# Kernel tuning notes

Hardware: AMD Instinct MI355X
Metric: run time of the kernel (lower is better)

## Reference

```python
import jax, jax.numpy as jnp
import numpy as np
import math

NEG = -1000000.0


def setup_inputs() -> dict:
    key = jax.random.key(0)
    ks = jax.random.split(key, 8)
    B, S, D = 4, 2048, 1024
    std = 1.0 / math.sqrt(D)
    return {
        "queries": jax.random.normal(ks[0], (B, S, D), jnp.float32),
        "keys": jax.random.normal(ks[1], (B, S, D), jnp.float32),
        "values": jax.random.normal(ks[2], (B, S, D), jnp.float32),
        "valid_len": jax.random.randint(ks[3], (B,), 1, S, dtype=jnp.int64 if jax.config.jax_enable_x64 else jnp.int32),
        "W_q": jax.random.normal(ks[4], (D, D), jnp.float32) * std,
        "W_k": jax.random.normal(ks[5], (D, D), jnp.float32) * std,
        "W_v": jax.random.normal(ks[6], (D, D), jnp.float32) * std,
        "W_o": jax.random.normal(ks[7], (D, D), jnp.float32) * std,
    }


def reference(queries, keys, values, valid_len, W_q, W_k, W_v, W_o):
    NUM_HEADS = 16
    B, S, D = queries.shape
    hd = D // NUM_HEADS

    def split_heads(x):
        # (B, S, D) -> (B, H, S, hd)
        return x.reshape(B, -1, NUM_HEADS, hd).transpose(0, 2, 1, 3)

    # nn.Linear with weight W applies x @ W.T
    q = split_heads(queries @ W_q.T)
    k = split_heads(keys @ W_k.T)
    v = split_heads(values @ W_v.T)

    scale = 1.0 / math.sqrt(hd)
    scores = jnp.einsum('bhqd,bhkd->bhqk', q, k) * scale  # (B, H, Sq, Sk)

    # key-padding mask from valid_len: positions >= valid_len are masked
    kpos = jnp.arange(scores.shape[-1])
    pad_mask = kpos[None, None, None, :] >= valid_len[:, None, None, None]
    scores = jnp.where(pad_mask, NEG, scores)
    attn = jax.nn.softmax(scores, axis=-1)

    out = jnp.einsum('bhqk,bhkd->bhqd', attn, v)  # (B, H, Sq, hd)
    out = out.transpose(0, 2, 1, 3).reshape(B, -1, D)
    return out @ W_o.T
```

## Files before the change

kernel.cpp:

```cpp
#include <hip/hip_runtime.h>
#include <hip/hip_bf16.h>

using bf16_t = __bf16;
using bf16x8 = __attribute__((ext_vector_type(8))) __bf16;
using bf16x4 = __attribute__((ext_vector_type(4))) __bf16;
using bf16x2 = __attribute__((ext_vector_type(2))) __bf16;
using f32x4  = __attribute__((ext_vector_type(4))) float;

#define S_  2048
#define D_  1024

typedef __attribute__((address_space(1))) unsigned int glb_u32;
typedef __attribute__((address_space(3))) unsigned int lds_u32;

__device__ __forceinline__ void async_cp16(const void* g, void* lds) {
    __builtin_amdgcn_global_load_lds(
        (glb_u32*)(unsigned long long)g,
        (lds_u32*)(unsigned int)(unsigned long long)lds,
        16, 0, 0);
}

__global__ __launch_bounds__(256) void cast_f32_bf16(const float* __restrict__ s,
                                                     bf16_t* __restrict__ d, int n4) {
    int i = blockIdx.x * 256 + threadIdx.x;
    if (i >= n4) return;
    float4 f = reinterpret_cast<const float4*>(s)[i];
    bf16x4 o;
    o[0] = (bf16_t)f.x; o[1] = (bf16_t)f.y; o[2] = (bf16_t)f.z; o[3] = (bf16_t)f.w;
    reinterpret_cast<bf16x4*>(d)[i] = o;
}

__global__ __launch_bounds__(256) void cast2_f32_bf16(const float* __restrict__ a, const float* __restrict__ b,
                                                      bf16_t* __restrict__ oa, bf16_t* __restrict__ ob, int n4) {
    int i = blockIdx.x * 256 + threadIdx.x;
    if (i >= n4) return;
    const float* s = blockIdx.y ? b : a;
    bf16_t*      d = blockIdx.y ? ob : oa;
    float4 f = reinterpret_cast<const float4*>(s)[i];
    bf16x4 o;
    o[0] = (bf16_t)f.x; o[1] = (bf16_t)f.y; o[2] = (bf16_t)f.z; o[3] = (bf16_t)f.w;
    reinterpret_cast<bf16x4*>(d)[i] = o;
}

__global__ __launch_bounds__(256) void cast4_f32_bf16(const float* __restrict__ a, const float* __restrict__ b,
                                                      const float* __restrict__ c, const float* __restrict__ dd,
                                                      bf16_t* __restrict__ oa, bf16_t* __restrict__ ob,
                                                      bf16_t* __restrict__ oc, bf16_t* __restrict__ od, int n4) {
    int i = blockIdx.x * 256 + threadIdx.x;
    if (i >= n4) return;
    const float* s; bf16_t* d;
    int w = blockIdx.y;
    if      (w == 0) { s = a;  d = oa; }
    else if (w == 1) { s = b;  d = ob; }
    else if (w == 2) { s = c;  d = oc; }
    else             { s = dd; d = od; }
    float4 f = reinterpret_cast<const float4*>(s)[i];
    bf16x4 o;
    o[0] = (bf16_t)f.x; o[1] = (bf16_t)f.y; o[2] = (bf16_t)f.z; o[3] = (bf16_t)f.w;
    reinterpret_cast<bf16x4*>(d)[i] = o;
}

template <int OUTMODE>
__global__ __launch_bounds__(256) void gemm_bt(const bf16_t* __restrict__ A,
                                               const bf16_t* __restrict__ Bt,
                                               void* __restrict__ Cv, float scale) {
    __shared__ bf16_t As[128 * 32];
    __shared__ bf16_t Bs[128 * 32];
    const int K = 1024;
    int tid  = threadIdx.x;
    int lane = tid & 63;
    int w    = tid >> 6;
    int l15  = lane & 15, quad = lane >> 4;
    int m0 = blockIdx.y * 128, n0 = blockIdx.x * 128;
    int wm = (w >> 1) * 64, wn = (w & 1) * 64;

    const bf16_t* Ag = A  + (size_t)(m0 + (tid >> 2)) * K + (tid & 3) * 8;
    const bf16_t* Bg = Bt + (size_t)(n0 + (tid >> 2)) * K + (tid & 3) * 8;
    bf16_t* Asw = As + tid * 8;
    bf16_t* Bsw = Bs + tid * 8;

    f32x4 acc[4][4] = {};

    for (int k0 = 0; k0 < K; k0 += 32) {
        __syncthreads();
        async_cp16(Ag + k0,                    Asw);
        async_cp16(Ag + k0 + (size_t)64 * K,   Asw + 2048);
        async_cp16(Bg + k0,                    Bsw);
        async_cp16(Bg + k0 + (size_t)64 * K,   Bsw + 2048);
        __syncthreads();
        bf16x8 af[4], bfr[4];
#pragma unroll
        for (int t = 0; t < 4; t++) {
            af[t]  = *reinterpret_cast<const bf16x8*>(&As[(wm + t * 16 + l15) * 32 + quad * 8]);
            bfr[t] = *reinterpret_cast<const bf16x8*>(&Bs[(wn + t * 16 + l15) * 32 + quad * 8]);
        }
#pragma unroll
        for (int mt = 0; mt < 4; mt++)
#pragma unroll
            for (int nt = 0; nt < 4; nt++)
                acc[mt][nt] = __builtin_amdgcn_mfma_f32_16x16x32_bf16(af[mt], bfr[nt], acc[mt][nt], 0, 0, 0);
    }

#pragma unroll
    for (int mt = 0; mt < 4; mt++)
#pragma unroll
        for (int nt = 0; nt < 4; nt++) {
            if (OUTMODE == 2) {
                int m = m0 + wm + mt * 16 + quad * 4;
                int n = n0 + wn + nt * 16 + l15;
                bf16x4 o4;
#pragma unroll
                for (int r = 0; r < 4; r++) o4[r] = (bf16_t)(acc[mt][nt][r] * scale);
                size_t vrow = (size_t)((m >> 11) * 16 + (n >> 6)) * 64 + (n & 63);
                *reinterpret_cast<bf16x4*>(&((bf16_t*)Cv)[vrow * S_ + (m & 2047)]) = o4;
            } else {
#pragma unroll
                for (int r = 0; r < 4; r++) {
                    int m = m0 + wm + mt * 16 + quad * 4 + r;
                    int n = n0 + wn + nt * 16 + l15;
                    size_t idx = (size_t)m * 1024 + n;
                    if (OUTMODE == 1) reinterpret_cast<float*>(Cv)[idx] = acc[mt][nt][r] * scale;
                    else              reinterpret_cast<bf16_t*>(Cv)[idx] = (bf16_t)(acc[mt][nt][r] * scale);
                }
            }
        }
}

__global__ __launch_bounds__(256) void attn_fused(const bf16_t* __restrict__ Qp,
                                                  const bf16_t* __restrict__ Kp,
                                                  const bf16_t* __restrict__ Vt,
                                                  const int* __restrict__ vlen_p,
                                                  bf16_t* __restrict__ Out) {
    __shared__ bf16_t smem[4][64 * 64];

    int tid  = threadIdx.x;
    int lane = tid & 63, w = tid >> 6;
    int l15  = lane & 15, quad = lane >> 4;

    int nk[4], ord[4] = {0, 1, 2, 3};
#pragma unroll
    for (int i = 0; i < 4; i++) nk[i] = (vlen_p[i] + 63) >> 6;
#pragma unroll
    for (int i = 0; i < 3; i++)
#pragma unroll
        for (int j = 0; j < 3 - i; j++)
            if (nk[ord[j + 1]] > nk[ord[j]]) { int t = ord[j]; ord[j] = ord[j + 1]; ord[j + 1] = t; }

    int bid  = blockIdx.x;
    int b    = ord[bid >> 9];
    int t    = bid & 511;
    int h    = (t & 7) * 2 + ((t >> 3) & 1);
    int qblk = t >> 4;
    int vlen = vlen_p[b];
    int nkb  = (vlen + 63) >> 6;

    const bf16_t* Qg = Qp + (size_t)(b * S_ + qblk * 64) * D_ + h * 64;
    const bf16_t* Kg = Kp + (size_t)b * S_ * D_ + h * 64;
    const bf16_t* Vg = Vt + (size_t)(b * 16 + h) * 64 * S_;

    auto stage = [&](const bf16_t* g, size_t rstride, bf16_t* lds) {
#pragma unroll
        for (int j = 0; j < 2; j++) {
            int linear = j * 256 + tid;
            int row = linear >> 3, s = linear & 7;
            async_cp16(g + (size_t)row * rstride + (s ^ (row & 7)) * 8, lds + linear * 8);
        }
    };

    stage(Qg, D_, smem[2]);
    stage(Kg, D_, smem[0]);
    stage(Vg, S_, smem[1]);
    __syncthreads();

    bf16x8 qf[2];
    {
        int row = w * 16 + l15, x = row & 7;
#pragma unroll
        for (int kk = 0; kk < 2; kk++)
            qf[kk] = *reinterpret_cast<const bf16x8*>(&smem[2][row * 64 + ((kk * 4 + quad) ^ x) * 8]);
    }
    __syncthreads();

    f32x4 o[4] = {};
    float l_st = 0.f;

    for (int kb = 0; kb < nkb; kb++) {
        int cur = kb & 1;
        if (kb + 1 < nkb) {
            int nxt = cur ^ 1;
            stage(Kg + (size_t)(kb + 1) * 64 * D_, D_, smem[nxt * 2]);
            stage(Vg + (kb + 1) * 64,              S_, smem[nxt * 2 + 1]);
        }
        const bf16_t* Kc = smem[cur * 2];
        const bf16_t* Vc = smem[cur * 2 + 1];

        f32x4 sc[4] = {};
#pragma unroll
        for (int nt = 0; nt < 4; nt++) {
            int row = nt * 16 + l15, x = row & 7;
#pragma unroll
            for (int kk = 0; kk < 2; kk++) {
                bf16x8 kf = *reinterpret_cast<const bf16x8*>(&Kc[row * 64 + ((kk * 4 + quad) ^ x) * 8]);
                sc[nt] = __builtin_amdgcn_mfma_f32_16x16x32_bf16(kf, qf[kk], sc[nt], 0, 0, 0);
            }
        }

        bool partial = (vlen & 63) && (kb == nkb - 1);
        bf16x8 pf[2];
        float lacc = 0.f;
        if (!partial) {
#pragma unroll
            for (int nt = 0; nt < 4; nt++)
#pragma unroll
                for (int r = 0; r < 4; r++) {
                    float p = __builtin_exp2f(sc[nt][r]);
                    lacc += p;
                    pf[nt >> 1][(nt & 1) * 4 + r] = (bf16_t)p;
                }
        } else {
#pragma unroll
            for (int nt = 0; nt < 4; nt++)
#pragma unroll
                for (int r = 0; r < 4; r++) {
                    float p = __builtin_exp2f(sc[nt][r]);
                    if (kb * 64 + nt * 16 + quad * 4 + r >= vlen) p = 0.f;
                    lacc += p;
                    pf[nt >> 1][(nt & 1) * 4 + r] = (bf16_t)p;
                }
        }
        l_st += lacc;

#pragma unroll
        for (int np = 0; np < 2; np++)
#pragma unroll
            for (int dt = 0; dt < 4; dt++) {
                int row = dt * 16 + l15, x = row & 7;
                int off = (quad & 1) * 4;
                bf16x4 v0 = *reinterpret_cast<const bf16x4*>(&Vc[row * 64 + (((np * 4)     + (quad >> 1)) ^ x) * 8 + off]);
                bf16x4 v1 = *reinterpret_cast<const bf16x4*>(&Vc[row * 64 + (((np * 4 + 2) + (quad >> 1)) ^ x) * 8 + off]);
                bf16x8 vf;
#pragma unroll
                for (int j = 0; j < 4; j++) { vf[j] = v0[j]; vf[4 + j] = v1[j]; }
                o[dt] = __builtin_amdgcn_mfma_f32_16x16x32_bf16(vf, pf[np], o[dt], 0, 0, 0);
            }

        __syncthreads();
    }

    float l = l_st;
    l += __shfl_xor(l, 16);
    l += __shfl_xor(l, 32);
    float inv = 1.0f / l;

    bf16_t* T = smem[0];
    {
        int row = w * 16 + l15, x = row & 7;
#pragma unroll
        for (int dt = 0; dt < 4; dt++) {
            bf16x4 o4;
#pragma unroll
            for (int r = 0; r < 4; r++) o4[r] = (bf16_t)(o[dt][r] * inv);
            int slot = dt * 2 + (quad >> 1);
            *reinterpret_cast<bf16x4*>(&T[row * 64 + (slot ^ x) * 8 + (quad & 1) * 4]) = o4;
        }
    }
    __syncthreads();
    {
        int row = tid >> 2, ch = tid & 3, x = row & 7;
        size_t obase = (size_t)(b * S_ + qblk * 64 + row) * D_ + h * 64 + ch * 16;
        bf16x8 f0 = *reinterpret_cast<const bf16x8*>(&T[row * 64 + ((ch * 2)     ^ x) * 8]);
        bf16x8 f1 = *reinterpret_cast<const bf16x8*>(&T[row * 64 + ((ch * 2 + 1) ^ x) * 8]);
        *reinterpret_cast<bf16x8*>(&Out[obase])     = f0;
        *reinterpret_cast<bf16x8*>(&Out[obase + 8]) = f1;
    }
}

extern "C" void kernel_launch(void* const* d_in, const int* in_sizes, int n_in,
                              void* d_out, int out_size, void* d_ws, size_t ws_size,
                              hipStream_t stream) {
    const float* q  = (const float*)d_in[0];
    const float* k  = (const float*)d_in[1];
    const float* v  = (const float*)d_in[2];
    const int*   vl = (const int*)d_in[3];
    const float* Wq = (const float*)d_in[4];
    const float* Wk = (const float*)d_in[5];
    const float* Wv = (const float*)d_in[6];
    const float* Wo = (const float*)d_in[7];
    float* out = (float*)d_out;

    bf16_t* ws = (bf16_t*)d_ws;
    const size_t SD = (size_t)8192 * 1024;
    const size_t WW = (size_t)1024 * 1024;
    bf16_t* tmpA = ws;
    bf16_t* tmpB = ws + SD;
    bf16_t* Qp   = ws + 2 * SD;
    bf16_t* Kp   = ws + 3 * SD;
    bf16_t* Vt   = ws + 4 * SD;
    bf16_t* Wqb  = ws + 5 * SD;
    bf16_t* Wkb  = Wqb + WW;
    bf16_t* Wvb  = Wqb + 2 * WW;
    bf16_t* Wob  = Wqb + 3 * WW;

    const float cs = 0.18033688f;
    dim3 blk(256);
    dim3 gg(8, 64);

    cast4_f32_bf16<<<dim3(1024, 4), blk, 0, stream>>>(Wq, Wk, Wv, Wo, Wqb, Wkb, Wvb, Wob, 262144);
    cast2_f32_bf16<<<dim3(8192, 2), blk, 0, stream>>>(q, k, tmpA, tmpB, 2097152);

    gemm_bt<0><<<gg, blk, 0, stream>>>(tmpA, Wqb, Qp, cs);
    gemm_bt<0><<<gg, blk, 0, stream>>>(tmpB, Wkb, Kp, 1.0f);
    cast_f32_bf16<<<dim3(8192), blk, 0, stream>>>(v, tmpA, 2097152);
    gemm_bt<2><<<gg, blk, 0, stream>>>(tmpA, Wvb, Vt, 1.0f);

    attn_fused<<<dim3(2048), blk, 0, stream>>>(Qp, Kp, Vt, vl, tmpB);
    gemm_bt<1><<<gg, blk, 0, stream>>>(tmpB, Wob, out, 1.0f);
}
```

Measured before the change: 355.5 us.

## Double-buffer GEMM tiles, remap blocks per XCD, permute V layout for vector loads

The projection GEMM now double-buffers its LDS tiles, prefetching the next K slice while computing the current one, with a single barrier per iteration. Block indices are remapped so that consecutive M tiles land on the same XCD, aiming for better L2 reuse. The transposed-V output permutes sequence positions within 32-element groups so the attention kernel can read each V fragment with one 16-byte LDS load instead of two 8-byte loads. The attention staging code also precomputes global pointers and advances them incrementally. This doubles the GEMM's LDS footprint and relies on the V permutation matching the P fragment ordering.

```diff
diff --git a/kernel.cpp b/kernel.cpp
--- a/kernel.cpp
+++ b/kernel.cpp
@@ -64,41 +64,52 @@
 __global__ __launch_bounds__(256) void gemm_bt(const bf16_t* __restrict__ A,
                                                const bf16_t* __restrict__ Bt,
                                                void* __restrict__ Cv, float scale) {
-    __shared__ bf16_t As[128 * 32];
-    __shared__ bf16_t Bs[128 * 32];
+    __shared__ bf16_t As[2][128 * 32];
+    __shared__ bf16_t Bs[2][128 * 32];
     const int K = 1024;
     int tid  = threadIdx.x;
     int lane = tid & 63;
     int w    = tid >> 6;
     int l15  = lane & 15, quad = lane >> 4;
-    int m0 = blockIdx.y * 128, n0 = blockIdx.x * 128;
+
+    int bid = blockIdx.y * gridDim.x + blockIdx.x;
+    int xcd = bid & 7, idx = bid >> 3;
+    int m0 = (xcd * 8 + (idx & 7)) * 128;
+    int n0 = (idx >> 3) * 128;
     int wm = (w >> 1) * 64, wn = (w & 1) * 64;
 
     const bf16_t* Ag = A  + (size_t)(m0 + (tid >> 2)) * K + (tid & 3) * 8;
     const bf16_t* Bg = Bt + (size_t)(n0 + (tid >> 2)) * K + (tid & 3) * 8;
-    bf16_t* Asw = As + tid * 8;
-    bf16_t* Bsw = Bs + tid * 8;
 
     f32x4 acc[4][4] = {};
 
+    async_cp16(Ag,                  &As[0][tid * 8]);
+    async_cp16(Ag + (size_t)64 * K, &As[0][tid * 8 + 2048]);
+    async_cp16(Bg,                  &Bs[0][tid * 8]);
+    async_cp16(Bg + (size_t)64 * K, &Bs[0][tid * 8 + 2048]);
+    __syncthreads();
+
     for (int k0 = 0; k0 < K; k0 += 32) {
-        __syncthreads();
-        async_cp16(Ag + k0,                    Asw);
-        async_cp16(Ag + k0 + (size_t)64 * K,   Asw + 2048);
-        async_cp16(Bg + k0,                    Bsw);
-        async_cp16(Bg + k0 + (size_t)64 * K,   Bsw + 2048);
-        __syncthreads();
+        int cur = (k0 >> 5) & 1;
+        if (k0 + 32 < K) {
+            int nxt = cur ^ 1;
+            async_cp16(Ag + k0 + 32,                  &As[nxt][tid * 8]);
+            async_cp16(Ag + k0 + 32 + (size_t)64 * K, &As[nxt][tid * 8 + 2048]);
+            async_cp16(Bg + k0 + 32,                  &Bs[nxt][tid * 8]);
+            async_cp16(Bg + k0 + 32 + (size_t)64 * K, &Bs[nxt][tid * 8 + 2048]);
+        }
         bf16x8 af[4], bfr[4];
 #pragma unroll
         for (int t = 0; t < 4; t++) {
-            af[t]  = *reinterpret_cast<const bf16x8*>(&As[(wm + t * 16 + l15) * 32 + quad * 8]);
-            bfr[t] = *reinterpret_cast<const bf16x8*>(&Bs[(wn + t * 16 + l15) * 32 + quad * 8]);
+            af[t]  = *reinterpret_cast<const bf16x8*>(&As[cur][(wm + t * 16 + l15) * 32 + quad * 8]);
+            bfr[t] = *reinterpret_cast<const bf16x8*>(&Bs[cur][(wn + t * 16 + l15) * 32 + quad * 8]);
         }
 #pragma unroll
         for (int mt = 0; mt < 4; mt++)
 #pragma unroll
             for (int nt = 0; nt < 4; nt++)
                 acc[mt][nt] = __builtin_amdgcn_mfma_f32_16x16x32_bf16(af[mt], bfr[nt], acc[mt][nt], 0, 0, 0);
+        __syncthreads();
     }
 
 #pragma unroll
@@ -112,15 +123,17 @@
 #pragma unroll
                 for (int r = 0; r < 4; r++) o4[r] = (bf16_t)(acc[mt][nt][r] * scale);
                 size_t vrow = (size_t)((m >> 11) * 16 + (n >> 6)) * 64 + (n & 63);
-                *reinterpret_cast<bf16x4*>(&((bf16_t*)Cv)[vrow * S_ + (m & 2047)]) = o4;
+                int ml = m & 2047;
+                int mp = (ml & ~31) | (((ml >> 2) & 3) << 3) | (((ml >> 4) & 1) << 2);
+                *reinterpret_cast<bf16x4*>(&((bf16_t*)Cv)[vrow * S_ + mp]) = o4;
             } else {
 #pragma unroll
                 for (int r = 0; r < 4; r++) {
                     int m = m0 + wm + mt * 16 + quad * 4 + r;
                     int n = n0 + wn + nt * 16 + l15;
-                    size_t idx = (size_t)m * 1024 + n;
-                    if (OUTMODE == 1) reinterpret_cast<float*>(Cv)[idx] = acc[mt][nt][r] * scale;
-                    else              reinterpret_cast<bf16_t*>(Cv)[idx] = (bf16_t)(acc[mt][nt][r] * scale);
+                    size_t idx2 = (size_t)m * 1024 + n;
+                    if (OUTMODE == 1) reinterpret_cast<float*>(Cv)[idx2] = acc[mt][nt][r] * scale;
+                    else              reinterpret_cast<bf16_t*>(Cv)[idx2] = (bf16_t)(acc[mt][nt][r] * scale);
                 }
             }
         }
@@ -158,18 +171,22 @@
     const bf16_t* Kg = Kp + (size_t)b * S_ * D_ + h * 64;
     const bf16_t* Vg = Vt + (size_t)(b * 16 + h) * 64 * S_;
 
-    auto stage = [&](const bf16_t* g, size_t rstride, bf16_t* lds) {
-#pragma unroll
-        for (int j = 0; j < 2; j++) {
-            int linear = j * 256 + tid;
-            int row = linear >> 3, s = linear & 7;
-            async_cp16(g + (size_t)row * rstride + (s ^ (row & 7)) * 8, lds + linear * 8);
-        }
-    };
-
-    stage(Qg, D_, smem[2]);
-    stage(Kg, D_, smem[0]);
-    stage(Vg, S_, smem[1]);
+    int r0 = tid >> 3, s0 = tid & 7;
+    int sx = (s0 ^ (r0 & 7)) * 8;
+    const bf16_t* kS0 = Kg + (size_t)r0 * D_ + sx;
+    const bf16_t* kS1 = kS0 + (size_t)32 * D_;
+    const bf16_t* vS0 = Vg + (size_t)r0 * S_ + sx;
+    const bf16_t* vS1 = vS0 + (size_t)32 * S_;
+
+    {
+        const bf16_t* qS0 = Qg + (size_t)r0 * D_ + sx;
+        async_cp16(qS0,                   smem[2] + tid * 8);
+        async_cp16(qS0 + (size_t)32 * D_, smem[2] + tid * 8 + 2048);
+        async_cp16(kS0, smem[0] + tid * 8);
+        async_cp16(kS1, smem[0] + tid * 8 + 2048);
+        async_cp16(vS0, smem[1] + tid * 8);
+        async_cp16(vS1, smem[1] + tid * 8 + 2048);
+    }
     __syncthreads();
 
     bf16x8 qf[2];
@@ -188,8 +205,12 @@
         int cur = kb & 1;
         if (kb + 1 < nkb) {
             int nxt = cur ^ 1;
-            stage(Kg + (size_t)(kb + 1) * 64 * D_, D_, smem[nxt * 2]);
-            stage(Vg + (kb + 1) * 64,              S_, smem[nxt * 2 + 1]);
+            kS0 += (size_t)64 * D_; kS1 += (size_t)64 * D_;
+            vS0 += 64;              vS1 += 64;
+            async_cp16(kS0, smem[nxt * 2]     + tid * 8);
+            async_cp16(kS1, smem[nxt * 2]     + tid * 8 + 2048);
+            async_cp16(vS0, smem[nxt * 2 + 1] + tid * 8);
+            async_cp16(vS1, smem[nxt * 2 + 1] + tid * 8 + 2048);
         }
         const bf16_t* Kc = smem[cur * 2];
         const bf16_t* Vc = smem[cur * 2 + 1];
@@ -235,12 +256,7 @@
 #pragma unroll
             for (int dt = 0; dt < 4; dt++) {
                 int row = dt * 16 + l15, x = row & 7;
-                int off = (quad & 1) * 4;
-                bf16x4 v0 = *reinterpret_cast<const bf16x4*>(&Vc[row * 64 + (((np * 4)     + (quad >> 1)) ^ x) * 8 + off]);
-                bf16x4 v1 = *reinterpret_cast<const bf16x4*>(&Vc[row * 64 + (((np * 4 + 2) + (quad >> 1)) ^ x) * 8 + off]);
-                bf16x8 vf;
-#pragma unroll
-                for (int j = 0; j < 4; j++) { vf[j] = v0[j]; vf[4 + j] = v1[j]; }
+                bf16x8 vf = *reinterpret_cast<const bf16x8*>(&Vc[row * 64 + ((np * 4 + quad) ^ x) * 8]);
                 o[dt] = __builtin_amdgcn_mfma_f32_16x16x32_bf16(vf, pf[np], o[dt], 0, 0, 0);
             }
 
```

Result: faster. 322.9 us (-9.2%).
